# Kernel tuning notes

Measured on AMD Instinct MI355X. Metric: run time of the kernel, lower is better.

## Reference

```python
import jax, jax.numpy as jnp
import numpy as np

B = 1048576
K = 10  # max set size for presence/absent letter sets
D = 8   # letter_embedding_dim
H = 256 # mlp_hidden_dim
TOTAL = (5 + 5) * D + 2 * D  # 96


def setup_inputs() -> dict:
    key = jax.random.key(0)
    ks = jax.random.split(key, 12)
    return {
        "guess_indices": jax.random.randint(ks[0], (B, 5), 0, 26),
        "constraint_indices": jax.random.randint(ks[1], (B, 5), 0, 27),
        "presence_idx": jax.random.randint(ks[2], (B, K), 0, 26),
        "presence_len": jax.random.randint(ks[3], (B,), 0, K + 1),
        "absent_idx": jax.random.randint(ks[4], (B, K), 0, 26),
        "absent_len": jax.random.randint(ks[5], (B,), 0, K + 1),
        "guess_table": jax.random.normal(ks[6], (26, D), dtype=jnp.float32),
        "constraint_table": jax.random.normal(ks[7], (27, D), dtype=jnp.float32),
        "W1": jax.random.normal(ks[8], (TOTAL, H), dtype=jnp.float32) * 0.1,
        "b1": jnp.zeros((H,), dtype=jnp.float32),
        "W2": jax.random.normal(ks[9], (H, 1), dtype=jnp.float32) * 0.1,
        "b2": jnp.zeros((1,), dtype=jnp.float32),
    }


def _masked_mean(table, idx, ln):
    # Segment-mean over padded letter sets; empty set -> zeros (matches aggregate_set).
    emb = table[idx]  # [B, K, D]
    mask = (jnp.arange(idx.shape[1])[None, :] < ln[:, None]).astype(emb.dtype)  # [B, K]
    s = jnp.einsum('bkd,bk->bd', emb, mask)
    denom = jnp.maximum(ln, 1).astype(emb.dtype)[:, None]
    return jnp.where(ln[:, None] > 0, s / denom, jnp.zeros_like(s))


def reference(guess_indices, constraint_indices, presence_idx, presence_len,
              absent_idx, absent_len, guess_table, constraint_table,
              W1, b1, W2, b2):
    bsz = guess_indices.shape[0]
    guess_flat = guess_table[guess_indices].reshape(bsz, -1)            # [B, 5*D]
    constraint_flat = constraint_table[constraint_indices].reshape(bsz, -1)  # [B, 5*D]
    presence_agg = _masked_mean(guess_table, presence_idx, presence_len)     # [B, D]
    absent_agg = _masked_mean(guess_table, absent_idx, absent_len)           # [B, D]
    combined = jnp.concatenate([guess_flat, constraint_flat, presence_agg, absent_agg], axis=1)
    # MLP (dropout is identity in eval mode)
    h = jax.nn.relu(combined @ W1 + b1)
    return h @ W2 + b2  # [B, 1]
```

## Files before the change

### kernel.cpp

```cpp
#include <hip/hip_runtime.h>

typedef __attribute__((ext_vector_type(8))) short short8;
typedef __attribute__((ext_vector_type(16))) float f32x16;
typedef __attribute__((ext_vector_type(2))) float f32x2;

#define WS_GT   0
#define WS_CT   256
#define WS_W1T  512

__device__ __forceinline__ unsigned short f2bf(float f) {
    unsigned int u = __float_as_uint(f);
    u = (u + 0x7fffu + ((u >> 16) & 1u)) >> 16;
    return (unsigned short)u;
}
__device__ __forceinline__ float bflo(unsigned int w) { return __uint_as_float(w << 16); }
__device__ __forceinline__ float bfhi(unsigned int w) { return __uint_as_float(w & 0xffff0000u); }

__global__ __launch_bounds__(256) void prep_kernel(
    const float* __restrict__ gt, const float* __restrict__ ct,
    const float* __restrict__ W1, unsigned short* __restrict__ ws)
{
    int tid = blockIdx.x * 256 + threadIdx.x;
    if (tid < 208) ws[WS_GT + tid] = f2bf(gt[tid]);
    if (tid < 216) ws[WS_CT + tid] = f2bf(ct[tid]);
    if (tid < 24576) {
        int kl  = tid >> 8;
        int col = tid & 255;
        int chunk = kl >> 3, j = kl & 7;
        int hi, kk;
        if (chunk < 5)        { hi = 0; kk = chunk; }
        else if (chunk < 10)  { hi = 1; kk = chunk - 5; }
        else if (chunk == 10) { hi = 0; kk = 5; }
        else                  { hi = 1; kk = 5; }
        int s = kk * 2 + hi;
        ws[WS_W1T + col * 104 + s * 8 + j] = f2bf(W1[kl * 256 + col]);
    }
}

__global__ __launch_bounds__(256, 2) void wordle_kernel(
    const int* __restrict__ gidx, const int* __restrict__ cidx,
    const int* __restrict__ pidx, const int* __restrict__ plen,
    const int* __restrict__ aidx, const int* __restrict__ alen,
    const float* __restrict__ b1, const float* __restrict__ W2,
    const float* __restrict__ b2, const unsigned short* __restrict__ ws,
    float* __restrict__ out, int tilesPerBlock)
{
    __shared__ unsigned short w1t[26624];
    __shared__ float outbuf[128];

    {
        const uint4* src = (const uint4*)(ws + WS_W1T);
        uint4* dst = (uint4*)w1t;
        int tid = threadIdx.x;
        #pragma unroll
        for (int i = 0; i < 13; ++i) dst[tid + i * 256] = src[tid + i * 256];
    }
    __syncthreads();

    const int lane = threadIdx.x & 63;
    const int wv   = threadIdx.x >> 6;
    const int l31  = lane & 31;
    const int hi   = lane >> 5;
    const unsigned short* gt = ws + WS_GT;
    const unsigned short* ct = ws + WS_CT;
    const unsigned short* tb = hi ? ct : gt;
    const float b2v = b2[0];

    float w2r[8], b1r[8];
    #pragma unroll
    for (int nt = 0; nt < 8; ++nt) {
        w2r[nt] = W2[nt * 32 + l31];
        b1r[nt] = b1[nt * 32 + l31];
    }

    int ip0, ip1, ip2, ip3, ip4;
    int s0, s1, s2, s3, s4, s5, s6, s7, s8, s9;
    int lenv;

#define LOADIDX(T) do {                                                     \
        const int r_ = (blockIdx.x * tilesPerBlock + (T)) * 128 + wv * 32 + l31; \
        const int* ip_ = (hi ? cidx : gidx) + r_ * 5;                       \
        ip0 = ip_[0]; ip1 = ip_[1]; ip2 = ip_[2]; ip3 = ip_[3]; ip4 = ip_[4]; \
        const int* si_ = (hi ? aidx : pidx) + r_ * 10;                      \
        s0 = si_[0]; s1 = si_[1]; s2 = si_[2]; s3 = si_[3]; s4 = si_[4];    \
        s5 = si_[5]; s6 = si_[6]; s7 = si_[7]; s8 = si_[8]; s9 = si_[9];    \
        lenv = (hi ? alen : plen)[r_];                                      \
    } while (0)

    LOADIDX(0);

    for (int t = 0; t < tilesPerBlock; ++t) {
        const int tile = blockIdx.x * tilesPerBlock + t;

        short8 a0 = *(const short8*)(tb + ip0 * 8);
        short8 a1 = *(const short8*)(tb + ip1 * 8);
        short8 a2 = *(const short8*)(tb + ip2 * 8);
        short8 a3 = *(const short8*)(tb + ip3 * 8);
        short8 a4 = *(const short8*)(tb + ip4 * 8);
        uint4 e0 = *(const uint4*)(gt + s0 * 8);
        uint4 e1 = *(const uint4*)(gt + s1 * 8);
        uint4 e2 = *(const uint4*)(gt + s2 * 8);
        uint4 e3 = *(const uint4*)(gt + s3 * 8);
        uint4 e4 = *(const uint4*)(gt + s4 * 8);
        uint4 e5 = *(const uint4*)(gt + s5 * 8);
        uint4 e6 = *(const uint4*)(gt + s6 * 8);
        uint4 e7 = *(const uint4*)(gt + s7 * 8);
        uint4 e8 = *(const uint4*)(gt + s8 * 8);
        uint4 e9 = *(const uint4*)(gt + s9 * 8);
        const int len = lenv;

        if (t + 1 < tilesPerBlock) LOADIDX(t + 1);

        short8 a5;
        {
            f32x2 m0 = {0.f, 0.f}, m1 = {0.f, 0.f}, m2 = {0.f, 0.f}, m3 = {0.f, 0.f};
            uint4 ev[10] = {e0,e1,e2,e3,e4,e5,e6,e7,e8,e9};
            #pragma unroll
            for (int k = 0; k < 10; ++k) {
                const float w = (k < len) ? 1.f : 0.f;
                const f32x2 wv2 = {w, w};
                f32x2 v0 = {bflo(ev[k].x), bfhi(ev[k].x)};
                f32x2 v1 = {bflo(ev[k].y), bfhi(ev[k].y)};
                f32x2 v2 = {bflo(ev[k].z), bfhi(ev[k].z)};
                f32x2 v3 = {bflo(ev[k].w), bfhi(ev[k].w)};
                m0 += wv2 * v0; m1 += wv2 * v1; m2 += wv2 * v2; m3 += wv2 * v3;
            }
            const float scl = (len > 0) ? (1.f / (float)len) : 0.f;
            a5[0] = (short)f2bf(m0[0] * scl); a5[1] = (short)f2bf(m0[1] * scl);
            a5[2] = (short)f2bf(m1[0] * scl); a5[3] = (short)f2bf(m1[1] * scl);
            a5[4] = (short)f2bf(m2[0] * scl); a5[5] = (short)f2bf(m2[1] * scl);
            a5[6] = (short)f2bf(m3[0] * scl); a5[7] = (short)f2bf(m3[1] * scl);
        }

        f32x16 acc[8];
        #pragma unroll
        for (int nt = 0; nt < 8; ++nt)
            #pragma unroll
            for (int r = 0; r < 16; ++r) acc[nt][r] = 0.f;

        #pragma unroll
        for (int kk = 0; kk < 6; ++kk) {
            const short8 av = (kk == 0) ? a0 : (kk == 1) ? a1 : (kk == 2) ? a2
                           : (kk == 3) ? a3 : (kk == 4) ? a4 : a5;
            const int s = kk * 2 + hi;
            #pragma unroll
            for (int nt = 0; nt < 8; ++nt) {
                const int col = nt * 32 + l31;
                short8 bv = *(const short8*)(&w1t[col * 104 + s * 8]);
                acc[nt] = __builtin_amdgcn_mfma_f32_32x32x16_bf16(av, bv, acc[nt], 0, 0, 0);
            }
        }

        f32x2 part2[8];
        #pragma unroll
        for (int i = 0; i < 8; ++i) { part2[i][0] = 0.f; part2[i][1] = 0.f; }
        #pragma unroll
        for (int nt = 0; nt < 8; ++nt) {
            const f32x2 w2v = {w2r[nt], w2r[nt]};
            const f32x2 b1v = {b1r[nt], b1r[nt]};
            const f32x2 z = {0.f, 0.f};
            #pragma unroll
            for (int i = 0; i < 8; ++i) {
                f32x2 h = {acc[nt][2 * i], acc[nt][2 * i + 1]};
                h = __builtin_elementwise_max(h + b1v, z);
                part2[i] += h * w2v;
            }
        }

        const int b_ = (l31 >> 4) & 1, c_ = (l31 >> 3) & 1,
                  d_ = (l31 >> 2) & 1, e_ = (l31 >> 1) & 1;
        f32x2 q1[4], q2[2], q3;
        float p4, p5;
        #pragma unroll
        for (int i = 0; i < 4; ++i) {
            f32x2 keep = b_ ? part2[4 + i] : part2[i];
            f32x2 send = b_ ? part2[i]     : part2[4 + i];
            f32x2 got;
            got[0] = __shfl_xor(send[0], 16, 64);
            got[1] = __shfl_xor(send[1], 16, 64);
            q1[i] = keep + got;
        }
        #pragma unroll
        for (int i = 0; i < 2; ++i) {
            f32x2 keep = c_ ? q1[2 + i] : q1[i];
            f32x2 send = c_ ? q1[i]     : q1[2 + i];
            f32x2 got;
            got[0] = __shfl_xor(send[0], 8, 64);
            got[1] = __shfl_xor(send[1], 8, 64);
            q2[i] = keep + got;
        }
        {
            f32x2 keep = d_ ? q2[1] : q2[0];
            f32x2 send = d_ ? q2[0] : q2[1];
            f32x2 got;
            got[0] = __shfl_xor(send[0], 4, 64);
            got[1] = __shfl_xor(send[1], 4, 64);
            q3 = keep + got;
        }
        {
            float keep = e_ ? q3[1] : q3[0];
            float send = e_ ? q3[0] : q3[1];
            p4 = keep + __shfl_xor(send, 2, 64);
        }
        p5 = p4 + __shfl_xor(p4, 1, 64);

        if (!(lane & 1)) {
            const int r = l31 >> 1;
            outbuf[wv * 32 + 4 * hi + (r & 3) + 8 * (r >> 2)] = p5 + b2v;
        }
        asm volatile("s_waitcnt lgkmcnt(0)" ::: "memory");
        if (lane < 32) {
            out[tile * 128 + wv * 32 + lane] = outbuf[wv * 32 + lane];
        }
    }
#undef LOADIDX
}

extern "C" void kernel_launch(void* const* d_in, const int* in_sizes, int n_in,
                              void* d_out, int out_size, void* d_ws, size_t ws_size,
                              hipStream_t stream) {
    const int*   gidx = (const int*)d_in[0];
    const int*   cidx = (const int*)d_in[1];
    const int*   pidx = (const int*)d_in[2];
    const int*   plen = (const int*)d_in[3];
    const int*   aidx = (const int*)d_in[4];
    const int*   alen = (const int*)d_in[5];
    const float* gt   = (const float*)d_in[6];
    const float* ct   = (const float*)d_in[7];
    const float* W1   = (const float*)d_in[8];
    const float* b1   = (const float*)d_in[9];
    const float* W2   = (const float*)d_in[10];
    const float* b2   = (const float*)d_in[11];
    float* out = (float*)d_out;
    unsigned short* ws = (unsigned short*)d_ws;

    const int B = in_sizes[0] / 5;
    prep_kernel<<<96, 256, 0, stream>>>(gt, ct, W1, ws);

    const int tilesTotal = B / 128;
    int tpb = 16;
    while (tpb > 1 && (tilesTotal % tpb)) tpb >>= 1;
    const int blocks = tilesTotal / tpb;
    wordle_kernel<<<blocks, 256, 0, stream>>>(gidx, cidx, pidx, plen, aidx, alen,
                                              b1, W2, b2, ws, out, tpb);
}
```

Measured before the change: 76.97 us.

## Split hidden dim across wave pairs and use persistent grid-stride blocks

Each tile shrinks to 64 rows. The two waves of a pair each compute half of the 256 hidden columns, keeping 4 accumulators instead of 8, and their partial outputs are combined through a double-buffered shared array after a block barrier. The grid becomes a fixed 768 persistent blocks that stride over tiles, and launch bounds rise to 3 blocks per CU. The smaller register footprint is meant to allow higher occupancy and better latency hiding for the gathers. In exchange, each wave pair now loads the same indices and gathers twice, and every tile adds a __syncthreads.

```diff
diff --git a/kernel.cpp b/kernel.cpp
--- a/kernel.cpp
+++ b/kernel.cpp
@@ -37,16 +37,16 @@
     }
 }
 
-__global__ __launch_bounds__(256, 2) void wordle_kernel(
+__global__ __launch_bounds__(256, 3) void wordle_kernel(
     const int* __restrict__ gidx, const int* __restrict__ cidx,
     const int* __restrict__ pidx, const int* __restrict__ plen,
     const int* __restrict__ aidx, const int* __restrict__ alen,
     const float* __restrict__ b1, const float* __restrict__ W2,
     const float* __restrict__ b2, const unsigned short* __restrict__ ws,
-    float* __restrict__ out, int tilesPerBlock)
+    float* __restrict__ out, int nTiles, int stride)
 {
     __shared__ unsigned short w1t[26624];
-    __shared__ float outbuf[128];
+    __shared__ float outbuf[2][128];
 
     {
         const uint4* src = (const uint4*)(ws + WS_W1T);
@@ -59,6 +59,8 @@
 
     const int lane = threadIdx.x & 63;
     const int wv   = threadIdx.x >> 6;
+    const int rg   = wv >> 1;
+    const int ch   = wv & 1;
     const int l31  = lane & 31;
     const int hi   = lane >> 5;
     const unsigned short* gt = ws + WS_GT;
@@ -66,11 +68,11 @@
     const unsigned short* tb = hi ? ct : gt;
     const float b2v = b2[0];
 
-    float w2r[8], b1r[8];
+    float w2r[4], b1r[4];
     #pragma unroll
-    for (int nt = 0; nt < 8; ++nt) {
-        w2r[nt] = W2[nt * 32 + l31];
-        b1r[nt] = b1[nt * 32 + l31];
+    for (int j = 0; j < 4; ++j) {
+        w2r[j] = W2[(ch * 4 + j) * 32 + l31];
+        b1r[j] = b1[(ch * 4 + j) * 32 + l31];
     }
 
     int ip0, ip1, ip2, ip3, ip4;
@@ -78,7 +80,7 @@
     int lenv;
 
 #define LOADIDX(T) do {                                                     \
-        const int r_ = (blockIdx.x * tilesPerBlock + (T)) * 128 + wv * 32 + l31; \
+        const int r_ = (T) * 64 + rg * 32 + l31;                            \
         const int* ip_ = (hi ? cidx : gidx) + r_ * 5;                       \
         ip0 = ip_[0]; ip1 = ip_[1]; ip2 = ip_[2]; ip3 = ip_[3]; ip4 = ip_[4]; \
         const int* si_ = (hi ? aidx : pidx) + r_ * 10;                      \
@@ -87,10 +89,10 @@
         lenv = (hi ? alen : plen)[r_];                                      \
     } while (0)
 
-    LOADIDX(0);
-
-    for (int t = 0; t < tilesPerBlock; ++t) {
-        const int tile = blockIdx.x * tilesPerBlock + t;
+    LOADIDX(blockIdx.x);
+
+    int it = 0;
+    for (int t = blockIdx.x; t < nTiles; t += stride, ++it) {
 
         short8 a0 = *(const short8*)(tb + ip0 * 8);
         short8 a1 = *(const short8*)(tb + ip1 * 8);
@@ -109,7 +111,7 @@
         uint4 e9 = *(const uint4*)(gt + s9 * 8);
         const int len = lenv;
 
-        if (t + 1 < tilesPerBlock) LOADIDX(t + 1);
+        if (t + stride < nTiles) LOADIDX(t + stride);
 
         short8 a5;
         {
@@ -132,11 +134,11 @@
             a5[6] = (short)f2bf(m3[0] * scl); a5[7] = (short)f2bf(m3[1] * scl);
         }
 
-        f32x16 acc[8];
-        #pragma unroll
-        for (int nt = 0; nt < 8; ++nt)
-            #pragma unroll
-            for (int r = 0; r < 16; ++r) acc[nt][r] = 0.f;
+        f32x16 acc[4];
+        #pragma unroll
+        for (int j = 0; j < 4; ++j)
+            #pragma unroll
+            for (int r = 0; r < 16; ++r) acc[j][r] = 0.f;
 
         #pragma unroll
         for (int kk = 0; kk < 6; ++kk) {
@@ -144,10 +146,10 @@
                            : (kk == 3) ? a3 : (kk == 4) ? a4 : a5;
             const int s = kk * 2 + hi;
             #pragma unroll
-            for (int nt = 0; nt < 8; ++nt) {
-                const int col = nt * 32 + l31;
+            for (int j = 0; j < 4; ++j) {
+                const int col = (ch * 4 + j) * 32 + l31;
                 short8 bv = *(const short8*)(&w1t[col * 104 + s * 8]);
-                acc[nt] = __builtin_amdgcn_mfma_f32_32x32x16_bf16(av, bv, acc[nt], 0, 0, 0);
+                acc[j] = __builtin_amdgcn_mfma_f32_32x32x16_bf16(av, bv, acc[j], 0, 0, 0);
             }
         }
 
@@ -155,13 +157,13 @@
         #pragma unroll
         for (int i = 0; i < 8; ++i) { part2[i][0] = 0.f; part2[i][1] = 0.f; }
         #pragma unroll
-        for (int nt = 0; nt < 8; ++nt) {
-            const f32x2 w2v = {w2r[nt], w2r[nt]};
-            const f32x2 b1v = {b1r[nt], b1r[nt]};
+        for (int j = 0; j < 4; ++j) {
+            const f32x2 w2v = {w2r[j], w2r[j]};
+            const f32x2 b1v = {b1r[j], b1r[j]};
             const f32x2 z = {0.f, 0.f};
             #pragma unroll
             for (int i = 0; i < 8; ++i) {
-                f32x2 h = {acc[nt][2 * i], acc[nt][2 * i + 1]};
+                f32x2 h = {acc[j][2 * i], acc[j][2 * i + 1]};
                 h = __builtin_elementwise_max(h + b1v, z);
                 part2[i] += h * w2v;
             }
@@ -206,11 +208,12 @@
 
         if (!(lane & 1)) {
             const int r = l31 >> 1;
-            outbuf[wv * 32 + 4 * hi + (r & 3) + 8 * (r >> 2)] = p5 + b2v;
-        }
-        asm volatile("s_waitcnt lgkmcnt(0)" ::: "memory");
-        if (lane < 32) {
-            out[tile * 128 + wv * 32 + lane] = outbuf[wv * 32 + lane];
+            outbuf[it & 1][ch * 64 + rg * 32 + 4 * hi + (r & 3) + 8 * (r >> 2)] = p5;
+        }
+        __syncthreads();
+        if (threadIdx.x < 64) {
+            out[t * 64 + threadIdx.x] =
+                outbuf[it & 1][threadIdx.x] + outbuf[it & 1][64 + threadIdx.x] + b2v;
         }
     }
 #undef LOADIDX
@@ -237,10 +240,8 @@
     const int B = in_sizes[0] / 5;
     prep_kernel<<<96, 256, 0, stream>>>(gt, ct, W1, ws);
 
-    const int tilesTotal = B / 128;
-    int tpb = 16;
-    while (tpb > 1 && (tilesTotal % tpb)) tpb >>= 1;
-    const int blocks = tilesTotal / tpb;
+    const int nTiles = B / 64;
+    const int blocks = 768;
     wordle_kernel<<<blocks, 256, 0, stream>>>(gidx, cidx, pidx, plen, aidx, alen,
-                                              b1, W2, b2, ws, out, tpb);
-}
+                                              b1, W2, b2, ws, out, nTiles, blocks);
+}
```

After: 121.2 us. 1.57x slower.
